# Performance work log

Hardware: AMD Instinct MI355X
Metric: run time of the kernel (lower is better)

The kernel has to match this reference:

```python
import jax
import jax.numpy as jnp
from jax import lax
import numpy as np

N_LEVELS = 4
NMS_THRESH = 0.7          # proposal_iou passed to batch_filter_by_nms
MIN_WH = 1.0              # config.prediction_min_width_height


def _box_iou(a, b):
    # a: [K,4], b: [K,4], corner format (y1,x1,y2,x2) -- IoU is order-agnostic
    area_a = (a[:, 2] - a[:, 0]) * (a[:, 3] - a[:, 1])
    area_b = (b[:, 2] - b[:, 0]) * (b[:, 3] - b[:, 1])
    lt = jnp.maximum(a[:, None, :2], b[None, :, :2])
    rb = jnp.minimum(a[:, None, 2:], b[None, :, 2:])
    wh = jnp.clip(rb - lt, 0.0)
    inter = wh[..., 0] * wh[..., 1]
    union = area_a[:, None] + area_b[None, :] - inter
    return inter / jnp.maximum(union, 1e-9)


def setup_inputs() -> dict:
    key = jax.random.key(0)
    k1, k2, k3, k4, k5, k6 = jax.random.split(key, 6)
    N = 250000
    logits = jax.random.normal(k1, (N, 2), dtype=jnp.float32)
    cy = jax.random.uniform(k2, (N,), minval=0.0, maxval=1024.0)
    cx = jax.random.uniform(k3, (N,), minval=0.0, maxval=1024.0)
    h = jax.random.uniform(k4, (N,), minval=8.0, maxval=208.0)
    w = jax.random.uniform(k5, (N,), minval=8.0, maxval=208.0)
    rois = jnp.stack([cy - h / 2, cx - w / 2, cy + h / 2, cx + w / 2], axis=1).astype(jnp.float32)
    levels = jax.random.randint(k6, (N,), 0, N_LEVELS, dtype=jnp.int32)
    return {"logits": logits, "rois": rois, "levels": levels,
            "n_pre_nms": 2000, "n_post_nms": 1000}


def _batch_filter_by_nms(logits, rois, levels, n_pre_nms, n_post_nms):
    scores = jax.nn.softmax(logits, axis=1)[:, 1]
    # per-level top-n_pre_nms (mirrors split + argsort(descending)[:n_pre_nms])
    cand_s, cand_i, cand_l = [], [], []
    for lvl in range(N_LEVELS):
        s_l = jnp.where(levels == lvl, scores, -jnp.inf)
        top_s, top_i = lax.top_k(s_l, n_pre_nms)
        cand_s.append(top_s)
        cand_i.append(top_i)
        cand_l.append(jnp.full((n_pre_nms,), lvl, dtype=jnp.int32))
    cand_scores = jnp.concatenate(cand_s)          # [K]
    cand_idx = jnp.concatenate(cand_i)             # [K]
    cand_levels = jnp.concatenate(cand_l)          # [K]
    cand_valid = jnp.isfinite(cand_scores)         # levels with < n_pre_nms anchors
    cand_rois = rois[cand_idx]                     # [K,4]
    K = cand_rois.shape[0]

    # level-shift so NMS is independent per level (batched-NMS trick)
    sep = jnp.max(cand_rois) + 1.0
    shifted = cand_rois + (cand_levels.astype(cand_rois.dtype) * sep)[:, None]

    # greedy NMS over all candidates, sorted globally by score
    order = jnp.argsort(-cand_scores)
    b = shifted[order]
    v = cand_valid[order]
    iou = _box_iou(b, b)                           # [K,K]
    idx_range = jnp.arange(K)

    def body(i, keep):
        row = lax.dynamic_index_in_dim(iou, i, 0, keepdims=False)
        ki = lax.dynamic_index_in_dim(keep, i, 0, keepdims=False)
        sup = (row > NMS_THRESH) & ki & (idx_range > i)
        return keep & ~sup

    keep = lax.fori_loop(0, K, body, v)

    # first n_post_nms kept, in score order (fixed-size, padded)
    pos = jnp.where(keep, idx_range, K)
    sorted_pos = jnp.sort(pos)[:n_post_nms]
    out_valid = sorted_pos < K
    sel = order[jnp.clip(sorted_pos, 0, K - 1)]    # indices into cand_* arrays

    out_rois = cand_rois[sel]
    out_logits = logits[cand_idx[sel]]
    out_levels = cand_levels[sel]

    # remove_small_boxes
    hs = out_rois[:, 2] - out_rois[:, 0]
    ws = out_rois[:, 3] - out_rois[:, 1]
    out_valid = out_valid & (hs >= MIN_WH) & (ws >= MIN_WH)

    out_rois = jnp.where(out_valid[:, None], out_rois, 0.0)
    out_logits = jnp.where(out_valid[:, None], out_logits, 0.0)
    out_levels = jnp.where(out_valid, out_levels, -1)
    return out_logits, out_rois, out_levels, out_valid


def reference(logits, rois, levels, n_pre_nms, n_post_nms):
    return _batch_filter_by_nms(logits, rois, levels, int(n_pre_nms), int(n_post_nms))
```

## Files before the change

### kernel.cpp

```cpp
#include <hip/hip_runtime.h>
#include <stdint.h>

typedef uint32_t u32;
typedef uint64_t u64;

#define NLVL 4
#define NPRE 2000
#define NPOST 1000
#define KPAD 8192
#define TIE_CAP 4096
#define NCHUNK 128

#define OFF_SBITS 0u
#define OFF_CTRL  (2u<<20)
#define OFF_RANK  ((2u<<20) + (4u<<10))
#define OFF_H1    ((2u<<20) + (36u<<10))
#define OFF_HM    ((2u<<20) + (40u<<10))
#define OFF_KEPT  ((2u<<20) + (48u<<10))
#define OFF_TIE   ((2u<<20) + (64u<<10))
#define OFF_CAND  ((2u<<20) + (192u<<10))
#define OFF_SHIFT ((2u<<20) + (256u<<10))
#define OFF_CAND2 ((2u<<20) + (384u<<10))
#define OFF_MASK  (3u<<20)
#define WS_NEED   ((size_t)(3u<<20) + (size_t)NCHUNK * KPAD * 8u)
#define MEMSET_BYTES ((44u<<10))

#define C_CANDCNT 0
#define C_KEPTCNT 1
#define C_SEPMAX  16
#define C_P       32
#define C_RANK    36
#define C_TIECNT  48

__device__ __forceinline__ u32 fmap(float f) {
  u32 u = __float_as_uint(f);
  return (u & 0x80000000u) ? ~u : (u | 0x80000000u);
}
__device__ __forceinline__ float funmap(u32 u) {
  u = (u & 0x80000000u) ? (u & 0x7FFFFFFFu) : ~u;
  return __uint_as_float(u);
}

__device__ __forceinline__ float xla_expf(float x) {
  const float kLog2e = 1.44269504088896341f;
  const float kC1 = 0.693359375f;
  const float kC2 = -2.12194440e-4f;
  const float kP0 = 1.9875691500e-4f;
  const float kP1 = 1.3981999507e-3f;
  const float kP2 = 8.3334519073e-3f;
  const float kP3 = 4.1665795894e-2f;
  const float kP4 = 1.6666665459e-1f;
  const float kP5 = 5.0000001201e-1f;
  float xc = fminf(fmaxf(x, -88.3762626647949f), 88.3762626647950f);
  float fx = floorf(fmaf(xc, kLog2e, 0.5f));
  float tmp = __fmul_rn(kC1, fx);
  float z = __fmul_rn(kC2, fx);
  float r = __fsub_rn(xc, tmp);
  r = __fsub_rn(r, z);
  float r2 = __fmul_rn(r, r);
  float y = fmaf(r, kP0, kP1);
  y = fmaf(y, r, kP2);
  y = fmaf(y, r, kP3);
  y = fmaf(y, r, kP4);
  y = fmaf(y, r, kP5);
  y = fmaf(y, r2, r);
  y = __fadd_rn(y, 1.0f);
  int n = (int)fx;
  float two_n = __int_as_float((n + 127) << 23);
  return fmaxf(__fmul_rn(y, two_n), x);
}

__device__ __forceinline__ bool suppress(float4 a, float4 b) {
  float aa = __fmul_rn(__fsub_rn(a.z, a.x), __fsub_rn(a.w, a.y));
  float ab = __fmul_rn(__fsub_rn(b.z, b.x), __fsub_rn(b.w, b.y));
  float lty = fmaxf(a.x, b.x);
  float ltx = fmaxf(a.y, b.y);
  float rby = fminf(a.z, b.z);
  float rbx = fminf(a.w, b.w);
  float why = fmaxf(__fsub_rn(rby, lty), 0.0f);
  float whx = fmaxf(__fsub_rn(rbx, ltx), 0.0f);
  float inter = __fmul_rn(why, whx);
  float uni = __fsub_rn(__fadd_rn(aa, ab), inter);
  float iou = inter / fmaxf(uni, 1e-9f);
  return iou > 0.7f;
}

__device__ __forceinline__ u64 makekey(u32 sbits, u32 lvl, u32 idx) {
  return ((u64)(0x7FFFFFFFu - sbits) << 20) | ((u64)lvl << 18) | (u64)idx;
}

__device__ __forceinline__ void rank_scan256(const u32* __restrict__ h, u32 target,
                                             int lane, u32* bin_out, u32* before_out) {
  u32 b0 = h[255 - 4 * lane];
  u32 b1 = h[254 - 4 * lane];
  u32 b2 = h[253 - 4 * lane];
  u32 b3 = h[252 - 4 * lane];
  u32 s = b0 + b1 + b2 + b3;
  u32 inc = s;
  for (int o = 1; o < 64; o <<= 1) {
    u32 v = (u32)__shfl_up((int)inc, o);
    if (lane >= o) inc += v;
  }
  u32 excl = inc - s;
  u32 tot = (u32)__shfl((int)inc, 63);
  if (tot < target) { *bin_out = 0xFFFFFFFFu; *before_out = 0u; return; }
  bool hit = (excl < target) && (excl + s >= target);
  u32 E = 0, before = 0;
  if (hit) {
    u32 cum = excl;
    if (cum + b0 >= target) { E = 255 - 4 * (u32)lane; before = cum; }
    else { cum += b0;
      if (cum + b1 >= target) { E = 254 - 4 * (u32)lane; before = cum; }
      else { cum += b1;
        if (cum + b2 >= target) { E = 253 - 4 * (u32)lane; before = cum; }
        else { cum += b2; E = 252 - 4 * (u32)lane; before = cum; }
      }
    }
  }
  u64 hb = __ballot(hit);
  int src = __ffsll((unsigned long long)hb) - 1;
  *bin_out = (u32)__shfl((int)E, src);
  *before_out = (u32)__shfl((int)before, src);
}

__global__ __launch_bounds__(512) void k_score_hist(const float2* __restrict__ logits,
                                                    const int* __restrict__ levels,
                                                    u32* __restrict__ sbits,
                                                    u32* __restrict__ hist1, int n) {
  __shared__ u32 lh[NLVL * 256];
  int tid = threadIdx.x;
  for (int p = tid; p < NLVL * 256; p += 512) lh[p] = 0;
  __syncthreads();
  int i = blockIdx.x * 512 + tid;
  if (i < n) {
    float2 lg = logits[i];
    float m = fmaxf(lg.x, lg.y);
    float e0 = xla_expf(__fsub_rn(lg.x, m));
    float e1 = xla_expf(__fsub_rn(lg.y, m));
    float s = e1 / __fadd_rn(e0, e1);
    u32 b = __float_as_uint(s);
    sbits[i] = b;
    int lv = levels[i];
    atomicAdd(&lh[lv * 256 + (int)((b >> 23) & 0xFFu)], 1u);
  }
  __syncthreads();
  for (int p = tid; p < NLVL * 256; p += 512) {
    u32 v = lh[p];
    if (v) atomicAdd(&hist1[p], v);
  }
}

__global__ __launch_bounds__(512) void k_hist_m(const u32* __restrict__ sbits,
                                                const int* __restrict__ levels,
                                                const u32* __restrict__ hist1,
                                                u32* __restrict__ histm, int n) {
  __shared__ u32 lh[NLVL * 256];
  __shared__ u32 sE[NLVL];
  int tid = threadIdx.x;
  int lane = tid & 63, w = tid >> 6;
  for (int p = tid; p < NLVL * 256; p += 512) lh[p] = 0;
  if (w < NLVL) {
    u32 E, bef;
    rank_scan256(hist1 + w * 256, NPRE, lane, &E, &bef);
    if (lane == 0) sE[w] = E;
  }
  __syncthreads();
  int i = blockIdx.x * 512 + tid;
  if (i < n) {
    u32 b = sbits[i];
    int lv = levels[i];
    if (((b >> 23) & 0xFFu) == sE[lv])
      atomicAdd(&lh[lv * 256 + (int)((b >> 15) & 0xFFu)], 1u);
  }
  __syncthreads();
  for (int p = tid; p < NLVL * 256; p += 512) {
    u32 v = lh[p];
    if (v) atomicAdd(&histm[p], v);
  }
}

__global__ __launch_bounds__(512) void k_compact(const u32* __restrict__ sbits,
                                                 const int* __restrict__ levels,
                                                 const u32* __restrict__ hist1,
                                                 const u32* __restrict__ histm,
                                                 u32* __restrict__ ctrl,
                                                 u64* __restrict__ cand,
                                                 u64* __restrict__ tie, int n) {
  __shared__ u32 wcnt[8], wtieS[8][4];
  __shared__ u32 wbase, tiebase[4];
  __shared__ u32 sP[NLVL], sRANK[NLVL];
  int tid = threadIdx.x;
  int wid = tid >> 6, lane = tid & 63;
  if (wid < NLVL) {
    u32 E, bef1;
    rank_scan256(hist1 + wid * 256, NPRE, lane, &E, &bef1);
    u32 P = 0xFFFFFFFFu, RK = 0;
    if (E != 0xFFFFFFFFu) {
      u32 R1 = NPRE - bef1;
      u32 M, bef2;
      rank_scan256(histm + wid * 256, R1, lane, &M, &bef2);
      P = (E << 8) | M;
      RK = R1 - bef2;
    }
    if (lane == 0) {
      sP[wid] = P; sRANK[wid] = RK;
      if (blockIdx.x == 0) { ctrl[C_P + wid] = P; ctrl[C_RANK + wid] = RK; }
    }
  }
  __syncthreads();
  int i = blockIdx.x * 512 + tid;
  bool act = i < n;
  u32 b = 0; int lv = 0; u32 P = 0xFFFFFFFEu;
  if (act) {
    b = sbits[i];
    lv = levels[i];
    P = sP[lv];
  }
  u32 K = b >> 15;
  bool iscand = act && (P == 0xFFFFFFFFu || K > P);
  bool istie  = act && !iscand && (K == P);
  u64 cb = __ballot(iscand);
  u64 t0 = __ballot(istie && lv == 0);
  u64 t1 = __ballot(istie && lv == 1);
  u64 t2 = __ballot(istie && lv == 2);
  u64 t3 = __ballot(istie && lv == 3);
  if (lane == 0) {
    wcnt[wid] = (u32)__popcll(cb);
    wtieS[wid][0] = (u32)__popcll(t0);
    wtieS[wid][1] = (u32)__popcll(t1);
    wtieS[wid][2] = (u32)__popcll(t2);
    wtieS[wid][3] = (u32)__popcll(t3);
  }
  __syncthreads();
  if (tid == 0) {
    u32 tot = 0;
#pragma unroll
    for (int w = 0; w < 8; ++w) tot += wcnt[w];
    wbase = tot ? atomicAdd(&ctrl[C_CANDCNT], tot) : 0u;
  }
  if (tid < 4) {
    u32 tt = 0;
#pragma unroll
    for (int w = 0; w < 8; ++w) tt += wtieS[w][tid];
    tiebase[tid] = tt ? atomicAdd(&ctrl[C_TIECNT + tid], tt) : 0u;
  }
  __syncthreads();
  u64 lm = (1ull << lane) - 1ull;
  if (iscand) {
    u32 pre = 0;
    for (int w = 0; w < wid; ++w) pre += wcnt[w];
    u32 pos = wbase + pre + (u32)__popcll(cb & lm);
    if (pos < (u32)KPAD) cand[pos] = makekey(b, (u32)lv, (u32)i);
  }
  if (istie) {
    u64 tb = (lv == 0) ? t0 : (lv == 1) ? t1 : (lv == 2) ? t2 : t3;
    u32 pre = 0;
    for (int w = 0; w < wid; ++w) pre += wtieS[w][lv];
    u32 pos = tiebase[lv] + pre + (u32)__popcll(tb & lm);
    if (pos < (u32)TIE_CAP) tie[lv * TIE_CAP + pos] = makekey(b, (u32)lv, (u32)i);
  }
}

__global__ void k_ties(u32* __restrict__ ctrl, u64* __restrict__ cand,
                       const u64* __restrict__ tie) {
  int lvl = blockIdx.x;
  int tid = threadIdx.x;
  if (ctrl[C_P + lvl] == 0xFFFFFFFFu) return;
  u32 need = ctrl[C_RANK + lvl];
  if (need == 0) return;
  u32 n = min(ctrl[C_TIECNT + lvl], (u32)TIE_CAP);
  u32 m = 2; while (m < n) m <<= 1;
  __shared__ u64 buf[TIE_CAP];
  for (u32 t = tid; t < m; t += 256)
    buf[t] = (t < n) ? tie[lvl * TIE_CAP + t] : ~0ull;
  __syncthreads();
  for (u32 k = 2; k <= m; k <<= 1) {
    for (u32 j = k >> 1; j > 0; j >>= 1) {
      for (u32 p = tid; p < m; p += 256) {
        u32 q = p ^ j;
        if (q > p) {
          u64 a = buf[p], b = buf[q];
          bool desc = (p & k) != 0;
          if (desc ? (a < b) : (a > b)) { buf[p] = b; buf[q] = a; }
        }
      }
      __syncthreads();
    }
  }
  u32 cnt = min(need, n);
  __shared__ u32 basep;
  if (tid == 0) basep = atomicAdd(&ctrl[C_CANDCNT], cnt);
  __syncthreads();
  for (u32 t = tid; t < cnt; t += 256) {
    if (basep + t < (u32)KPAD) cand[basep + t] = buf[t];
  }
}

__global__ __launch_bounds__(256) void k_rankp(const u64* __restrict__ cand,
                                               const u32* __restrict__ ctrl,
                                               const float4* __restrict__ rois,
                                               u32* __restrict__ rankbuf,
                                               u32* __restrict__ ctrlw) {
  __shared__ u64 tilek[256];
  int tid = threadIdx.x;
  u32 g = blockIdx.x, h = blockIdx.y;
  u32 total = min(ctrl[C_CANDCNT], (u32)KPAD);
  u32 gid = g * 256 + (u32)tid;
  u64 mykey = (gid < total) ? cand[gid] : ~0ull;
  if (h == 0) {
    u32 mx = 0;
    if (gid < total) {
      u32 idx = (u32)(mykey & 0x3FFFFu);
      float4 r = rois[idx];
      mx = max(max(fmap(r.x), fmap(r.y)), max(fmap(r.z), fmap(r.w)));
    }
    for (int o = 32; o; o >>= 1) {
      u32 v = (u32)__shfl_xor((int)mx, o);
      mx = max(mx, v);
    }
    if ((tid & 63) == 0 && mx) atomicMax(&ctrlw[C_SEPMAX], mx);
  }
  u32 jbeg = h * 1024;
  if (jbeg >= total) return;
  u32 jend = min(jbeg + 1024, total);
  u32 cnt = 0;
  for (u32 base = jbeg; base < jend; base += 256) {
    u32 n = min(256u, jend - base);
    __syncthreads();
    if ((u32)tid < n) tilek[tid] = cand[base + (u32)tid];
    __syncthreads();
    if (n == 256u) {
#pragma unroll 8
      for (u32 j = 0; j < 256u; ++j) cnt += (tilek[j] < mykey) ? 1u : 0u;
    } else {
      for (u32 j = 0; j < n; ++j) cnt += (tilek[j] < mykey) ? 1u : 0u;
    }
  }
  if (gid < total && cnt) atomicAdd(&rankbuf[gid], cnt);
}

__global__ __launch_bounds__(256) void k_scatter(const u64* __restrict__ cand,
                                                 const u32* __restrict__ rankbuf,
                                                 const u32* __restrict__ ctrl,
                                                 const float4* __restrict__ rois,
                                                 u64* __restrict__ cand2,
                                                 float4* __restrict__ shifted) {
  u32 gid = blockIdx.x * 256 + threadIdx.x;
  u32 total = min(ctrl[C_CANDCNT], (u32)KPAD);
  if (gid >= total) return;
  u64 mykey = cand[gid];
  u32 rank = rankbuf[gid];
  cand2[rank] = mykey;
  float sep = __fadd_rn(funmap(ctrl[C_SEPMAX]), 1.0f);
  u32 idx = (u32)(mykey & 0x3FFFFu);
  u32 lvl = (u32)((mykey >> 18) & 3u);
  float4 r = rois[idx];
  float sh = __fmul_rn((float)lvl, sep);
  float4 o;
  o.x = __fadd_rn(r.x, sh);
  o.y = __fadd_rn(r.y, sh);
  o.z = __fadd_rn(r.z, sh);
  o.w = __fadd_rn(r.w, sh);
  shifted[rank] = o;
}

__global__ __launch_bounds__(256) void k_build(const float4* __restrict__ shifted,
                                               u64* __restrict__ maskT2) {
  u32 rb = blockIdx.y;
  u32 cb = blockIdx.x * 4 + (threadIdx.x >> 6);
  if (blockIdx.x * 4 + 3 < rb) return;
  int lane = threadIdx.x & 63;
  __shared__ float4 rbox[64];
  if (threadIdx.x < 64) rbox[threadIdx.x] = shifted[rb * 64 + threadIdx.x];
  __syncthreads();
  if (cb < rb) return;
  u32 jg = cb * 64 + (u32)lane;
  float4 myc = shifted[jg];
  u64 bits = 0;
  for (int s = 0; s < 64; ++s) {
    if ((rb * 64 + (u32)s) < jg && suppress(rbox[s], myc)) bits |= (1ull << s);
  }
  maskT2[(u64)rb * KPAD + jg] = bits;
}

__global__ __launch_bounds__(512) void k_scan(const u64* __restrict__ maskT2,
                                              const u64* __restrict__ cand2,
                                              u32* __restrict__ ctrl,
                                              const float2* __restrict__ logits,
                                              const float4* __restrict__ rois,
                                              float* __restrict__ out) {
  __shared__ u64 keptm[NCHUNK];
  __shared__ u64 pre[2][8];
  __shared__ u32 lkept[NPOST];
  __shared__ u32 keptS;
  int tid = threadIdx.x;
  int lane = tid & 63, w = tid >> 6;
  u32 total = min(ctrl[C_CANDCNT], (u32)KPAD);
  u32 chunks = (total + 63) >> 6;
  for (int p = tid; p < NCHUNK; p += 512) keptm[p] = 0;
  if (tid < 8)  pre[0][tid] = 0;
  if (tid >= 8 && tid < 16) pre[1][tid - 8] = 0;
  if (tid == 0) keptS = 0;
  __syncthreads();
  u32 kept = 0;
  u64 keepPrev = 0, lastWord = 0, diagCur = 0;
  if (w == 0 && chunks > 0) diagCur = maskT2[(u64)lane];
  for (u32 c = 0; c < chunks; ++c) {
    if (w == 0) {
      u64 nDiag = 0, nLast = 0;
      if (c + 1 < chunks) {
        nDiag = maskT2[(u64)(c + 1) * KPAD + (u64)(c + 1) * 64 + (u64)lane];
        nLast = maskT2[(u64)c * KPAD + (u64)(c + 1) * 64 + (u64)lane];
      }
      u64 remc = pre[c & 1][1] | pre[c & 1][2] | pre[c & 1][3] | pre[c & 1][4] |
                 pre[c & 1][5] | pre[c & 1][6] | pre[c & 1][7];
      remc |= __ballot((lastWord & keepPrev) != 0ull);
      u64 wv = ~remc;
      u32 rem2 = total - c * 64;
      if (rem2 < 64) wv &= ((1ull << rem2) - 1ull);
      u64 keep = wv;
      for (int it = 0; it < 64; ++it) {
        bool sup = (diagCur & keep) != 0ull;
        u64 nk = wv & ~__ballot(sup);
        if (nk == keep) break;
        keep = nk;
      }
      u32 pos = kept + (u32)__popcll(keep & ((1ull << lane) - 1ull));
      if (((keep >> lane) & 1ull) && pos < NPOST) lkept[pos] = c * 64 + (u32)lane;
      if (lane == 0) { keptm[c] = keep; keptS = kept + (u32)__popcll(keep); }
      keepPrev = keep;
      lastWord = nLast;
      diagCur = nDiag;
    } else {
      u64 a0 = 0, a1 = 0;
      if (c + 1 < chunks) {
        const u64* colbase = maskT2 + (u64)(c + 1) * 64 + (u64)lane;
        u32 ci = (u32)(w - 1);
        for (; ci + 7 < c; ci += 14) {
          u64 x0 = colbase[(u64)ci * KPAD] & keptm[ci];
          u64 x1 = colbase[(u64)(ci + 7) * KPAD] & keptm[ci + 7];
          a0 |= x0; a1 |= x1;
        }
        for (; ci < c; ci += 7) a0 |= colbase[(u64)ci * KPAD] & keptm[ci];
      }
      u64 bal = __ballot((a0 | a1) != 0ull);
      if (lane == 0) pre[(c + 1) & 1][w] = bal;
    }
    __syncthreads();
    kept = keptS;
    if (kept >= NPOST) break;
  }
  if (tid == 0) ctrl[C_KEPTCNT] = min(kept, (u32)NPOST);
  __syncthreads();
  u32 kn = min(kept, (u32)NPOST);
  for (u32 r = (u32)tid; r < NPOST; r += 512) {
    float l0 = 0.f, l1 = 0.f, b0 = 0.f, b1 = 0.f, b2 = 0.f, b3 = 0.f;
    float lvf = -1.0f, vf = 0.0f;
    if (r < kn) {
      u32 pos = lkept[r];
      u64 a = cand2[pos];
      u32 idx = (u32)(a & 0x3FFFFu);
      u32 lvl = (u32)((a >> 18) & 3u);
      float4 rb = rois[idx];
      float hs = __fsub_rn(rb.z, rb.x);
      float wsz = __fsub_rn(rb.w, rb.y);
      if (hs >= 1.0f && wsz >= 1.0f) {
        float2 lg = logits[idx];
        l0 = lg.x; l1 = lg.y;
        b0 = rb.x; b1 = rb.y; b2 = rb.z; b3 = rb.w;
        lvf = (float)lvl; vf = 1.0f;
      }
    }
    out[2 * r] = l0;
    out[2 * r + 1] = l1;
    out[2 * NPOST + 4 * r + 0] = b0;
    out[2 * NPOST + 4 * r + 1] = b1;
    out[2 * NPOST + 4 * r + 2] = b2;
    out[2 * NPOST + 4 * r + 3] = b3;
    out[6 * NPOST + r] = lvf;
    out[7 * NPOST + r] = vf;
  }
}

__global__ __launch_bounds__(1024) void k_nms(const float4* __restrict__ shifted,
                                              u32* __restrict__ ctrl, u32* __restrict__ keptpos) {
  __shared__ float4 kbox[NPOST];
  __shared__ u32 wflag[16];
  int tid = threadIdx.x;
  u32 total = min(ctrl[C_CANDCNT], (u32)KPAD);
  int n = 0;
  for (u32 i = 0; i < total; ++i) {
    float4 cur = shifted[i];
    bool sup = false;
    if (tid < n) sup = suppress(kbox[tid], cur);
    int any = __any(sup);
    if ((tid & 63) == 0) wflag[tid >> 6] = (u32)any;
    __syncthreads();
    u32 f = 0;
#pragma unroll
    for (int w = 0; w < 16; ++w) f |= wflag[w];
    if (!f) {
      if (tid == 0) { kbox[n] = cur; keptpos[n] = i; }
      ++n;
    }
    __syncthreads();
    if (n >= NPOST) break;
  }
  if (tid == 0) ctrl[C_KEPTCNT] = (u32)n;
}

__global__ void k_out(const u64* __restrict__ cand, const u32* __restrict__ keptpos,
                      const u32* __restrict__ ctrl, const float2* __restrict__ logits,
                      const float4* __restrict__ rois, float* __restrict__ out) {
  int r = blockIdx.x * blockDim.x + threadIdx.x;
  if (r >= NPOST) return;
  u32 kn = ctrl[C_KEPTCNT];
  float l0 = 0.f, l1 = 0.f, r0 = 0.f, r1 = 0.f, r2 = 0.f, r3 = 0.f;
  float lvf = -1.0f, vf = 0.0f;
  if (r < (int)kn) {
    u32 pos = keptpos[r];
    u64 a = cand[pos];
    u32 idx = (u32)(a & 0x3FFFFu);
    u32 lvl = (u32)((a >> 18) & 3u);
    float4 rb = rois[idx];
    float hs = __fsub_rn(rb.z, rb.x);
    float wsz = __fsub_rn(rb.w, rb.y);
    if (hs >= 1.0f && wsz >= 1.0f) {
      float2 lg = logits[idx];
      l0 = lg.x; l1 = lg.y;
      r0 = rb.x; r1 = rb.y; r2 = rb.z; r3 = rb.w;
      lvf = (float)lvl; vf = 1.0f;
    }
  }
  out[2 * r] = l0;
  out[2 * r + 1] = l1;
  out[2 * NPOST + 4 * r + 0] = r0;
  out[2 * NPOST + 4 * r + 1] = r1;
  out[2 * NPOST + 4 * r + 2] = r2;
  out[2 * NPOST + 4 * r + 3] = r3;
  out[6 * NPOST + r] = lvf;
  out[7 * NPOST + r] = vf;
}

extern "C" void kernel_launch(void* const* d_in, const int* in_sizes, int n_in,
                              void* d_out, int out_size, void* d_ws, size_t ws_size,
                              hipStream_t stream) {
  const float* logits = (const float*)d_in[0];
  const float* rois = (const float*)d_in[1];
  const int* levels = (const int*)d_in[2];
  int N = in_sizes[2];

  char* ws = (char*)d_ws;
  u32* sbits = (u32*)(ws + OFF_SBITS);
  u32* ctrl = (u32*)(ws + OFF_CTRL);
  u32* rankbuf = (u32*)(ws + OFF_RANK);
  u32* hist1 = (u32*)(ws + OFF_H1);
  u32* histm = (u32*)(ws + OFF_HM);
  u32* keptpos = (u32*)(ws + OFF_KEPT);
  u64* tie = (u64*)(ws + OFF_TIE);
  u64* cand = (u64*)(ws + OFF_CAND);
  float4* shifted = (float4*)(ws + OFF_SHIFT);
  u64* cand2 = (u64*)(ws + OFF_CAND2);
  u64* maskT2 = (u64*)(ws + OFF_MASK);

  hipMemsetAsync(ctrl, 0, MEMSET_BYTES, stream);

  int nb2 = (N + 511) / 512;
  k_score_hist<<<nb2, 512, 0, stream>>>((const float2*)logits, levels, sbits, hist1, N);
  k_hist_m<<<nb2, 512, 0, stream>>>(sbits, levels, hist1, histm, N);
  k_compact<<<nb2, 512, 0, stream>>>(sbits, levels, hist1, histm, ctrl, cand, tie, N);
  k_ties<<<NLVL, 256, 0, stream>>>(ctrl, cand, tie);
  {
    dim3 g(KPAD / 256, 8);
    k_rankp<<<g, 256, 0, stream>>>(cand, ctrl, (const float4*)rois, rankbuf, ctrl);
  }
  k_scatter<<<KPAD / 256, 256, 0, stream>>>(cand, rankbuf, ctrl, (const float4*)rois,
                                            cand2, shifted);
  if (ws_size >= WS_NEED) {
    dim3 g(KPAD / 256, KPAD / 64);
    k_build<<<g, 256, 0, stream>>>((const float4*)shifted, maskT2);
    k_scan<<<1, 512, 0, stream>>>(maskT2, cand2, ctrl,
                                  (const float2*)logits, (const float4*)rois, (float*)d_out);
  } else {
    k_nms<<<1, 1024, 0, stream>>>(shifted, ctrl, keptpos);
    k_out<<<(NPOST + 255) / 256, 256, 0, stream>>>(cand2, keptpos, ctrl, (const float2*)logits,
                                                   (const float4*)rois, (float*)d_out);
  }
}
```

Baseline: 125.8 us.

## Register-block IoU mask build: 4 columns per lane, precomputed areas, division-free test

The mask-building kernel now runs one 64-lane wavefront per block, and each lane handles four candidate columns. Each row box loaded from shared memory is therefore reused four times, and box areas are computed once per box instead of once per pair. The IoU > 0.7 test drops the float division and instead compares inter against a double-precision threshold times the union. The per-pair diagonal branch is replaced by a bitmask applied only on the diagonal block. The double-precision compare carries some cost on this hardware and could differ from the rounded-division result in edge cases.

```diff
diff --git a/kernel.cpp b/kernel.cpp
--- a/kernel.cpp
+++ b/kernel.cpp
@@ -31,6 +31,8 @@
 #define C_P       32
 #define C_RANK    36
 #define C_TIECNT  48
+
+#define MID 0x1.666667p-1
 
 __device__ __forceinline__ u32 fmap(float f) {
   u32 u = __float_as_uint(f);
@@ -85,6 +87,19 @@
   return iou > 0.7f;
 }
 
+__device__ __forceinline__ bool sup_fast(float ra, float4 r, float ca, float4 c) {
+  float lty = fmaxf(r.x, c.x);
+  float ltx = fmaxf(r.y, c.y);
+  float rby = fminf(r.z, c.z);
+  float rbx = fminf(r.w, c.w);
+  float why = fmaxf(__fsub_rn(rby, lty), 0.0f);
+  float whx = fmaxf(__fsub_rn(rbx, ltx), 0.0f);
+  float inter = __fmul_rn(why, whx);
+  float uni = __fsub_rn(__fadd_rn(ra, ca), inter);
+  float den = fmaxf(uni, 1e-9f);
+  return (double)inter >= MID * (double)den;
+}
+
 __device__ __forceinline__ u64 makekey(u32 sbits, u32 lvl, u32 idx) {
   return ((u64)(0x7FFFFFFFu - sbits) << 20) | ((u64)lvl << 18) | (u64)idx;
 }
@@ -364,23 +379,44 @@
   shifted[rank] = o;
 }
 
-__global__ __launch_bounds__(256) void k_build(const float4* __restrict__ shifted,
-                                               u64* __restrict__ maskT2) {
+__global__ __launch_bounds__(64) void k_build(const float4* __restrict__ shifted,
+                                              u64* __restrict__ maskT2) {
   u32 rb = blockIdx.y;
-  u32 cb = blockIdx.x * 4 + (threadIdx.x >> 6);
-  if (blockIdx.x * 4 + 3 < rb) return;
-  int lane = threadIdx.x & 63;
+  u32 cq = blockIdx.x;
+  if (cq * 4 + 3 < rb) return;
+  int lane = threadIdx.x;
   __shared__ float4 rbox[64];
-  if (threadIdx.x < 64) rbox[threadIdx.x] = shifted[rb * 64 + threadIdx.x];
-  __syncthreads();
-  if (cb < rb) return;
-  u32 jg = cb * 64 + (u32)lane;
-  float4 myc = shifted[jg];
-  u64 bits = 0;
+  __shared__ float rarea[64];
+  float4 rv = shifted[rb * 64 + (u32)lane];
+  rbox[lane] = rv;
+  rarea[lane] = __fmul_rn(__fsub_rn(rv.z, rv.x), __fsub_rn(rv.w, rv.y));
+  __syncthreads();
+  u32 j0 = cq * 256 + (u32)lane;
+  float4 c0 = shifted[j0];
+  float4 c1 = shifted[j0 + 64];
+  float4 c2 = shifted[j0 + 128];
+  float4 c3 = shifted[j0 + 192];
+  float a0 = __fmul_rn(__fsub_rn(c0.z, c0.x), __fsub_rn(c0.w, c0.y));
+  float a1 = __fmul_rn(__fsub_rn(c1.z, c1.x), __fsub_rn(c1.w, c1.y));
+  float a2 = __fmul_rn(__fsub_rn(c2.z, c2.x), __fsub_rn(c2.w, c2.y));
+  float a3 = __fmul_rn(__fsub_rn(c3.z, c3.x), __fsub_rn(c3.w, c3.y));
+  u64 b0 = 0, b1 = 0, b2 = 0, b3 = 0;
+#pragma unroll 8
   for (int s = 0; s < 64; ++s) {
-    if ((rb * 64 + (u32)s) < jg && suppress(rbox[s], myc)) bits |= (1ull << s);
-  }
-  maskT2[(u64)rb * KPAD + jg] = bits;
+    float4 r = rbox[s];
+    float ra = rarea[s];
+    b0 |= (u64)sup_fast(ra, r, a0, c0) << s;
+    b1 |= (u64)sup_fast(ra, r, a1, c1) << s;
+    b2 |= (u64)sup_fast(ra, r, a2, c2) << s;
+    b3 |= (u64)sup_fast(ra, r, a3, c3) << s;
+  }
+  u64 diagm = (1ull << lane) - 1ull;
+  u32 cb = cq * 4;
+  u64* dst = maskT2 + (u64)rb * KPAD + (u64)cb * 64 + (u64)lane;
+  if (cb >= rb)     dst[0]   = (cb == rb)     ? (b0 & diagm) : b0;
+  if (cb + 1 >= rb) dst[64]  = (cb + 1 == rb) ? (b1 & diagm) : b1;
+  if (cb + 2 >= rb) dst[128] = (cb + 2 == rb) ? (b2 & diagm) : b2;
+  if (cb + 3 >= rb) dst[192] = (cb + 3 == rb) ? (b3 & diagm) : b3;
 }
 
 __global__ __launch_bounds__(512) void k_scan(const u64* __restrict__ maskT2,
@@ -578,7 +614,7 @@
                                             cand2, shifted);
   if (ws_size >= WS_NEED) {
     dim3 g(KPAD / 256, KPAD / 64);
-    k_build<<<g, 256, 0, stream>>>((const float4*)shifted, maskT2);
+    k_build<<<g, 64, 0, stream>>>((const float4*)shifted, maskT2);
     k_scan<<<1, 512, 0, stream>>>(maskT2, cand2, ctrl,
                                   (const float2*)logits, (const float4*)rois, (float*)d_out);
   } else {
```

Result: faster. 110.9 us (-11.8%).
